# Optimization experiments

Hardware: AMD Instinct MI355X
Metric: run time of the kernel (lower is better)

The kernel has to match this reference:

```python
import jax, jax.numpy as jnp
import numpy as np

B, T, C, H = 4, 1024, 2048, 16
HD = C // H  # head_dim = 128


def setup_inputs() -> dict:
    key = jax.random.key(0)
    k1, k2, k3 = jax.random.split(key, 3)
    x = jax.random.normal(k1, (B, T, C), dtype=jnp.float32)
    # torch Linear weights are [out_features, in_features]
    w_attn = jax.random.normal(k2, (3 * C, C), dtype=jnp.float32) * 0.02
    w_proj = jax.random.normal(k3, (C, C), dtype=jnp.float32) * 0.02
    attention_mask = jnp.ones((B, T), dtype=jnp.int32)  # 1 = attend, 0 = padded
    return {"x": x, "w_attn": w_attn, "w_proj": w_proj, "attention_mask": attention_mask}


def reference(x, w_attn, w_proj, attention_mask):
    b, t, c = x.shape
    hd = c // H
    # fused QKV projection: [B,T,3C] -> [3,B,H,T,hd]
    qkv = jnp.einsum("btc,fc->btf", x, w_attn)
    qkv = qkv.reshape(b, t, 3, H, hd).transpose(2, 0, 3, 1, 4)
    q, k, v = qkv[0], qkv[1], qkv[2]
    # padding mask -> additive bias, broadcast over heads and query positions
    bias = jnp.where(attention_mask == 0, -jnp.inf, 0.0).astype(x.dtype)[:, None, None, :]
    scale = 1.0 / jnp.sqrt(jnp.asarray(hd, dtype=x.dtype))
    att = jnp.einsum("bhqd,bhkd->bhqk", q, k) * scale + bias
    att = jax.nn.softmax(att, axis=-1)  # dropout_p=0 (eval mode)
    y = jnp.einsum("bhqk,bhkd->bhqd", att, v)
    y = y.transpose(0, 2, 1, 3).reshape(b, t, c)
    return jnp.einsum("btc,oc->bto", y, w_proj)
```

## Files before the change

kernel.cpp:

```cpp
#include <hip/hip_runtime.h>
#include <hip/hip_bf16.h>

#define NB   4
#define NH   16
#define SEQ  1024
#define CH   2048
#define HDIM 128

typedef float f32x4 __attribute__((ext_vector_type(4)));
typedef short short8 __attribute__((ext_vector_type(8)));

static __device__ __forceinline__ unsigned short f2bf(float f) {
  unsigned u = __builtin_bit_cast(unsigned, f);
  u += 0x7FFFu + ((u >> 16) & 1u);
  return (unsigned short)(u >> 16);
}

#define GLOAD16(g, l)                                                        \
  __builtin_amdgcn_global_load_lds(                                          \
      (const __attribute__((address_space(1))) void*)(g),                    \
      (__attribute__((address_space(3))) void*)(l), 16, 0, 0)

__global__ __launch_bounds__(256)
void cast_bf16(const float* __restrict__ in, unsigned short* __restrict__ out, int n4) {
  int i = blockIdx.x * 256 + threadIdx.x;
  int stride = gridDim.x * 256;
  for (; i < n4; i += stride) {
    float4 v = ((const float4*)in)[i];
    ushort4 o;
    o.x = f2bf(v.x); o.y = f2bf(v.y); o.z = f2bf(v.z); o.w = f2bf(v.w);
    ((ushort4*)out)[i] = o;
  }
}

__device__ __forceinline__ void gemm_core_glds(
    const unsigned short* __restrict__ A, const unsigned short* __restrict__ B,
    int K, int m0, int n0, short* As, short* Bs, f32x4 acc[4][4]) {
  const int tid = threadIdx.x, lane = tid & 63, wid = tid >> 6;
  const int wr = wid >> 1, wc = wid & 1, lr = lane & 15, lg = lane >> 4;
  const int sr = lane >> 3;
  const int sk = (lane & 7) * 8;

  for (int k0 = 0; k0 < K; k0 += 64) {
    __syncthreads();
#pragma unroll
    for (int p = 0; p < 4; ++p) {
      int c = wid * 4 + p;
      GLOAD16(A + (size_t)(m0 + c * 8 + sr) * K + k0 + sk, As + c * 512);
      GLOAD16(B + (size_t)(n0 + c * 8 + sr) * K + k0 + sk, Bs + c * 512);
    }
    __syncthreads();
#pragma unroll
    for (int kc = 0; kc < 2; ++kc) {
      short8 af[4], bf[4];
#pragma unroll
      for (int f = 0; f < 4; ++f) {
        af[f] = *(const short8*)(As + (wr * 64 + f * 16 + lr) * 64 + kc * 32 + lg * 8);
        bf[f] = *(const short8*)(Bs + (wc * 64 + f * 16 + lr) * 64 + kc * 32 + lg * 8);
      }
#pragma unroll
      for (int fm = 0; fm < 4; ++fm)
#pragma unroll
        for (int fn = 0; fn < 4; ++fn)
          acc[fm][fn] = __builtin_amdgcn_mfma_f32_16x16x32_bf16(af[fm], bf[fn], acc[fm][fn], 0, 0, 0);
    }
  }
  __syncthreads();
}

__global__ __launch_bounds__(256)
void gemm_qkv_bf16(const unsigned short* __restrict__ xb, const unsigned short* __restrict__ wab,
                   unsigned short* __restrict__ Qb, unsigned short* __restrict__ Kb,
                   unsigned short* __restrict__ Vtb) {
  __shared__ short smem[17408];
  short* As = smem;
  short* Bs = smem + 8192;
  f32x4 acc[4][4];
#pragma unroll
  for (int i = 0; i < 4; ++i)
#pragma unroll
    for (int j = 0; j < 4; ++j) acc[i][j] = (f32x4){0.f, 0.f, 0.f, 0.f};

  const int m0 = blockIdx.y * 128, n0 = blockIdx.x * 128;
  gemm_core_glds(xb, wab, CH, m0, n0, As, Bs, acc);

  const int tid = threadIdx.x, lane = tid & 63, wid = tid >> 6;
  const int wr = wid >> 1, wc = wid & 1, lr = lane & 15, lg = lane >> 4;
  const int which = n0 >> 11;
  const int h = (n0 >> 7) & 15;
  const int bb = m0 >> 10, t0 = m0 & 1023;

  if (which < 2) {
    unsigned short* dst0 = (which == 0) ? Qb : Kb;
    const float sc = (which == 0) ? 0.08838834764831843f : 1.0f;
#pragma unroll
    for (int fm = 0; fm < 4; ++fm)
#pragma unroll
      for (int fn = 0; fn < 4; ++fn)
#pragma unroll
        for (int r = 0; r < 4; ++r)
          smem[(wr * 64 + fm * 16 + lg * 4 + r) * 136 + wc * 64 + fn * 16 + lr] =
              (short)f2bf(acc[fm][fn][r] * sc);
    __syncthreads();
    int row = tid >> 1, sg = tid & 1;
    unsigned short* dst = dst0 + (((size_t)(bb * NH + h)) * SEQ + t0 + row) * HDIM + sg * 64;
    const short* src = smem + row * 136 + sg * 64;
#pragma unroll
    for (int j = 0; j < 8; ++j)
      *(uint4*)(dst + j * 8) = *(const uint4*)(src + j * 8);
  } else {
#pragma unroll
    for (int fm = 0; fm < 4; ++fm)
#pragma unroll
      for (int fn = 0; fn < 4; ++fn)
#pragma unroll
        for (int r = 0; r < 4; ++r)
          smem[(wc * 64 + fn * 16 + lr) * 136 + wr * 64 + fm * 16 + lg * 4 + r] =
              (short)f2bf(acc[fm][fn][r]);
    __syncthreads();
    int dd = tid >> 1, sg = tid & 1;
    unsigned short* gdst = Vtb + (((size_t)(bb * NH + h)) * HDIM + dd) * SEQ + t0 + sg * 64;
    const short* src = smem + dd * 136 + sg * 64;
#pragma unroll
    for (int j = 0; j < 8; ++j)
      *(uint4*)(gdst + j * 8) = *(const uint4*)(src + j * 8);
  }
}

__global__ __launch_bounds__(256)
void gemm_proj_bf16(const unsigned short* __restrict__ Yb, const unsigned short* __restrict__ wpb,
                    float* __restrict__ out) {
  __shared__ short smem[17408];
  short* As = smem;
  short* Bs = smem + 8192;
  f32x4 acc[4][4];
#pragma unroll
  for (int i = 0; i < 4; ++i)
#pragma unroll
    for (int j = 0; j < 4; ++j) acc[i][j] = (f32x4){0.f, 0.f, 0.f, 0.f};

  const int m0 = blockIdx.y * 128, n0 = blockIdx.x * 128;
  gemm_core_glds(Yb, wpb, CH, m0, n0, As, Bs, acc);

  const int tid = threadIdx.x, lane = tid & 63, wid = tid >> 6;
  const int wr = wid >> 1, wc = wid & 1, lr = lane & 15, lg = lane >> 4;
  float* fb = (float*)smem;
  for (int p = 0; p < 2; ++p) {
    if (wr == p) {
#pragma unroll
      for (int fm = 0; fm < 4; ++fm)
#pragma unroll
        for (int fn = 0; fn < 4; ++fn)
#pragma unroll
          for (int r = 0; r < 4; ++r)
            fb[(fm * 16 + lg * 4 + r) * 132 + wc * 64 + fn * 16 + lr] = acc[fm][fn][r];
    }
    __syncthreads();
    int row = tid >> 2, seg = tid & 3;
    float* dst = out + (size_t)(m0 + p * 64 + row) * CH + n0 + seg * 32;
    const float* src = fb + row * 132 + seg * 32;
#pragma unroll
    for (int j = 0; j < 8; ++j)
      *(uint4*)(dst + j * 4) = *(const uint4*)(src + j * 4);
    __syncthreads();
  }
}

__global__ __launch_bounds__(256)
void attn_mfma(const unsigned short* __restrict__ Qb, const unsigned short* __restrict__ Kb,
               const unsigned short* __restrict__ Vtb, const int* __restrict__ mask,
               unsigned short* __restrict__ Yb) {
  __shared__ short asmem[12032];
  short* Kls = asmem;
  short* Vls = asmem + 4352;
  short* Pls = asmem + 9472;
  const int tid = threadIdx.x, lane = tid & 63, wid = tid >> 6;
  const int lr = lane & 15, lg = lane >> 4;
  const int bh = blockIdx.y, b = bh >> 4, h = bh & 15;
  const int q0 = blockIdx.x * 64 + wid * 16;

  short8 qf[4];
  const unsigned short* qptr = Qb + ((size_t)bh * SEQ + q0 + lr) * HDIM + lg * 8;
#pragma unroll
  for (int dc = 0; dc < 4; ++dc) qf[dc] = *(const short8*)(qptr + dc * 32);

  f32x4 O[8];
#pragma unroll
  for (int i = 0; i < 8; ++i) O[i] = (f32x4){0.f, 0.f, 0.f, 0.f};
  float mrow[4] = {-3.0e38f, -3.0e38f, -3.0e38f, -3.0e38f};
  float lrow[4] = {0.f, 0.f, 0.f, 0.f};

  const unsigned short* kbase = Kb + (size_t)bh * SEQ * HDIM;
  const unsigned short* vbase = Vtb + (size_t)bh * HDIM * SEQ;
  short* Pw = Pls + wid * (16 * 40);
  const int* maskrow = mask + b * SEQ;

  for (int kt = 0; kt < SEQ; kt += 32) {
    __syncthreads();
    {
      int r = tid >> 3, s = tid & 7;
      const unsigned short* g = kbase + (size_t)(kt + r) * HDIM + s * 16;
      uint4 u0 = *(const uint4*)g, u1 = *(const uint4*)(g + 8);
      *(uint4*)(Kls + r * 136 + s * 16) = u0;
      *(uint4*)(Kls + r * 136 + s * 16 + 8) = u1;
      int d = tid >> 1, s2 = tid & 1;
      const unsigned short* gv = vbase + (size_t)d * SEQ + kt + s2 * 16;
      uint4 v0 = *(const uint4*)gv, v1 = *(const uint4*)(gv + 8);
      *(uint4*)(Vls + d * 40 + s2 * 16) = v0;
      *(uint4*)(Vls + d * 40 + s2 * 16 + 8) = v1;
    }
    __syncthreads();

    f32x4 s0 = (f32x4){0.f, 0.f, 0.f, 0.f}, s1 = (f32x4){0.f, 0.f, 0.f, 0.f};
#pragma unroll
    for (int dc = 0; dc < 4; ++dc) {
      short8 k0f = *(const short8*)(Kls + lr * 136 + dc * 32 + lg * 8);
      short8 k1f = *(const short8*)(Kls + (16 + lr) * 136 + dc * 32 + lg * 8);
      s0 = __builtin_amdgcn_mfma_f32_16x16x32_bf16(qf[dc], k0f, s0, 0, 0, 0);
      s1 = __builtin_amdgcn_mfma_f32_16x16x32_bf16(qf[dc], k1f, s1, 0, 0, 0);
    }

    float b0 = maskrow[kt + lr] ? 0.f : -1.0e30f;
    float b1 = maskrow[kt + 16 + lr] ? 0.f : -1.0e30f;
    float corr[4];
#pragma unroll
    for (int r = 0; r < 4; ++r) {
      float a0 = s0[r] + b0, a1 = s1[r] + b1;
      float tm = fmaxf(a0, a1);
      tm = fmaxf(tm, __shfl_xor(tm, 1));
      tm = fmaxf(tm, __shfl_xor(tm, 2));
      tm = fmaxf(tm, __shfl_xor(tm, 4));
      tm = fmaxf(tm, __shfl_xor(tm, 8));
      float mn = fmaxf(mrow[r], tm);
      corr[r] = __expf(mrow[r] - mn);
      float p0 = __expf(a0 - mn), p1 = __expf(a1 - mn);
      mrow[r] = mn;
      float rs = p0 + p1;
      rs += __shfl_xor(rs, 1);
      rs += __shfl_xor(rs, 2);
      rs += __shfl_xor(rs, 4);
      rs += __shfl_xor(rs, 8);
      lrow[r] = lrow[r] * corr[r] + rs;
      Pw[(lg * 4 + r) * 40 + lr] = (short)f2bf(p0);
      Pw[(lg * 4 + r) * 40 + 16 + lr] = (short)f2bf(p1);
    }
#pragma unroll
    for (int db = 0; db < 8; ++db)
#pragma unroll
      for (int r = 0; r < 4; ++r) O[db][r] *= corr[r];

    short8 pa = *(const short8*)(Pw + lr * 40 + lg * 8);
#pragma unroll
    for (int db = 0; db < 8; ++db) {
      short8 vb = *(const short8*)(Vls + (db * 16 + lr) * 40 + lg * 8);
      O[db] = __builtin_amdgcn_mfma_f32_16x16x32_bf16(pa, vb, O[db], 0, 0, 0);
    }
  }

  float inv[4];
#pragma unroll
  for (int r = 0; r < 4; ++r) inv[r] = 1.0f / lrow[r];

  short* Ols = asmem;
  __syncthreads();
#pragma unroll
  for (int db = 0; db < 8; ++db)
#pragma unroll
    for (int r = 0; r < 4; ++r)
      Ols[(wid * 16 + lg * 4 + r) * 136 + db * 16 + lr] = (short)f2bf(O[db][r] * inv[r]);
  __syncthreads();
  {
    int row = tid >> 2, seg = tid & 3;
    unsigned short* dst =
        Yb + ((size_t)(b * SEQ + blockIdx.x * 64 + row)) * CH + h * HDIM + seg * 32;
    const short* src = Ols + row * 136 + seg * 32;
#pragma unroll
    for (int j = 0; j < 4; ++j)
      *(uint4*)(dst + j * 8) = *(const uint4*)(src + j * 8);
  }
}

extern "C" void kernel_launch(void* const* d_in, const int* in_sizes, int n_in,
                              void* d_out, int out_size, void* d_ws, size_t ws_size,
                              hipStream_t stream) {
  const float* x      = (const float*)d_in[0];
  const float* w_attn = (const float*)d_in[1];
  const float* w_proj = (const float*)d_in[2];
  const int*   mask   = (const int*)d_in[3];
  float* out = (float*)d_out;

  char* ws = (char*)d_ws;
  unsigned short* xb  = (unsigned short*)(ws);
  unsigned short* wab = (unsigned short*)(ws + 16777216);
  unsigned short* wpb = (unsigned short*)(ws + 41943040);
  unsigned short* Qb  = (unsigned short*)(ws + 50331648);
  unsigned short* Kb  = (unsigned short*)(ws + 67108864);
  unsigned short* Vtb = (unsigned short*)(ws + 83886080);
  unsigned short* Yb  = (unsigned short*)(ws + 100663296);

  cast_bf16<<<2048, 256, 0, stream>>>(x, xb, (NB * SEQ * CH) / 4);
  cast_bf16<<<2048, 256, 0, stream>>>(w_attn, wab, (3 * CH * CH) / 4);
  cast_bf16<<<2048, 256, 0, stream>>>(w_proj, wpb, (CH * CH) / 4);

  gemm_qkv_bf16<<<dim3(3 * CH / 128, NB * SEQ / 128), 256, 0, stream>>>(xb, wab, Qb, Kb, Vtb);
  attn_mfma<<<dim3(SEQ / 64, NB * NH), 256, 0, stream>>>(Qb, Kb, Vtb, mask, Yb);
  gemm_proj_bf16<<<dim3(CH / 128, NB * SEQ / 128), 256, 0, stream>>>(Yb, wpb, out);
}
```

Before: 470.6 us.

## Replace QKV GEMM with 256x256 double-buffered tile kernel and block swizzle

The QKV projection now uses a new kernel with 256x256 output tiles and 512 threads (8 waves, 8x4 MFMA fragments each). A/B tiles are staged with direct global-to-LDS loads into two LDS buffers, so the next K-slice is fetched while the current one is computed. A linear block-index swizzle groups neighbouring tiles for better L2 reuse. Larger tiles cut global/LDS traffic per FLOP. In exchange the kernel uses 128KB of LDS (one block per CU), launches only 384 blocks, which may leave a partial wave, and the epilogue runs in two serialized halves.

```diff
diff --git a/kernel.cpp b/kernel.cpp
--- a/kernel.cpp
+++ b/kernel.cpp
@@ -33,6 +33,119 @@
   }
 }
 
+__global__ __launch_bounds__(512, 2)
+void gemm_qkv_256(const unsigned short* __restrict__ xb, const unsigned short* __restrict__ wab,
+                  unsigned short* __restrict__ Qb, unsigned short* __restrict__ Kb,
+                  unsigned short* __restrict__ Vtb) {
+  __shared__ short smem[65536];
+  const int tid = threadIdx.x, lane = tid & 63, wid = tid >> 6;
+  const int wr = wid >> 2, wc = wid & 3, lr = lane & 15, lg = lane >> 4;
+  const int sr = lane >> 3, sk = (lane & 7) * 8;
+
+  const int lid = blockIdx.y * 24 + blockIdx.x;
+  const int swz = (lid & 7) * 48 + (lid >> 3);
+  const int bx = swz % 24, by = swz / 24;
+  const int m0 = by * 256, n0 = bx * 256;
+
+  f32x4 acc[8][4];
+#pragma unroll
+  for (int i = 0; i < 8; ++i)
+#pragma unroll
+    for (int j = 0; j < 4; ++j) acc[i][j] = (f32x4){0.f, 0.f, 0.f, 0.f};
+
+#define STAGE_TILE(b, k0)                                                      \
+  do {                                                                         \
+    short* As_ = smem + (b) * 32768;                                           \
+    short* Bs_ = As_ + 16384;                                                  \
+    _Pragma("unroll")                                                          \
+    for (int p = 0; p < 4; ++p) {                                              \
+      int c = wid * 4 + p;                                                     \
+      GLOAD16(xb + (size_t)(m0 + c * 8 + sr) * CH + (k0) + sk, As_ + c * 512); \
+      GLOAD16(wab + (size_t)(n0 + c * 8 + sr) * CH + (k0) + sk, Bs_ + c * 512);\
+    }                                                                          \
+  } while (0)
+
+  STAGE_TILE(0, 0);
+  __syncthreads();
+  int cur = 0;
+  for (int kt = 0; kt < 32; ++kt) {
+    if (kt + 1 < 32) STAGE_TILE(cur ^ 1, (kt + 1) * 64);
+    const short* As = smem + cur * 32768;
+    const short* Bs = As + 16384;
+#pragma unroll
+    for (int kc = 0; kc < 2; ++kc) {
+      short8 bfr[4];
+#pragma unroll
+      for (int fn = 0; fn < 4; ++fn)
+        bfr[fn] = *(const short8*)(Bs + (wc * 64 + fn * 16 + lr) * 64 + kc * 32 + lg * 8);
+#pragma unroll
+      for (int fm = 0; fm < 8; ++fm) {
+        short8 af = *(const short8*)(As + (wr * 128 + fm * 16 + lr) * 64 + kc * 32 + lg * 8);
+#pragma unroll
+        for (int fn = 0; fn < 4; ++fn)
+          acc[fm][fn] = __builtin_amdgcn_mfma_f32_16x16x32_bf16(af, bfr[fn], acc[fm][fn], 0, 0, 0);
+      }
+    }
+    __syncthreads();
+    cur ^= 1;
+  }
+#undef STAGE_TILE
+
+  const int which = n0 >> 11;
+  const int h0 = (n0 & 2047) >> 7;
+  const int bb = m0 >> 10, t0 = m0 & 1023;
+
+  if (which < 2) {
+    unsigned short* dst0 = (which == 0) ? Qb : Kb;
+    const float sc = (which == 0) ? 0.08838834764831843f : 1.0f;
+    for (int p = 0; p < 2; ++p) {
+      if (wr == p) {
+#pragma unroll
+        for (int fm = 0; fm < 8; ++fm)
+#pragma unroll
+          for (int fn = 0; fn < 4; ++fn)
+#pragma unroll
+            for (int r = 0; r < 4; ++r)
+              smem[(fm * 16 + lg * 4 + r) * 264 + wc * 64 + fn * 16 + lr] =
+                  (short)f2bf(acc[fm][fn][r] * sc);
+      }
+      __syncthreads();
+      int row = tid >> 2, seg = tid & 3;
+      int h = h0 + (seg >> 1), d0 = (seg & 1) * 64;
+      unsigned short* dst =
+          dst0 + (((size_t)(bb * NH + h)) * SEQ + t0 + p * 128 + row) * HDIM + d0;
+      const short* src = smem + row * 264 + seg * 64;
+#pragma unroll
+      for (int j = 0; j < 8; ++j)
+        *(uint4*)(dst + j * 8) = *(const uint4*)(src + j * 8);
+      __syncthreads();
+    }
+  } else {
+    for (int p = 0; p < 2; ++p) {
+      if (wr == p) {
+#pragma unroll
+        for (int fm = 0; fm < 8; ++fm)
+#pragma unroll
+          for (int fn = 0; fn < 4; ++fn)
+#pragma unroll
+            for (int r = 0; r < 4; ++r)
+              smem[(wc * 64 + fn * 16 + lr) * 136 + fm * 16 + lg * 4 + r] =
+                  (short)f2bf(acc[fm][fn][r]);
+      }
+      __syncthreads();
+      int d = tid >> 1, sg = tid & 1;
+      int h = h0 + (d >> 7), dl = d & 127;
+      unsigned short* dst =
+          Vtb + (((size_t)(bb * NH + h)) * HDIM + dl) * SEQ + t0 + p * 128 + sg * 64;
+      const short* src = smem + d * 136 + sg * 64;
+#pragma unroll
+      for (int j = 0; j < 8; ++j)
+        *(uint4*)(dst + j * 8) = *(const uint4*)(src + j * 8);
+      __syncthreads();
+    }
+  }
+}
+
 __device__ __forceinline__ void gemm_core_glds(
     const unsigned short* __restrict__ A, const unsigned short* __restrict__ B,
     int K, int m0, int n0, short* As, short* Bs, f32x4 acc[4][4]) {
@@ -66,65 +179,6 @@
     }
   }
   __syncthreads();
-}
-
-__global__ __launch_bounds__(256)
-void gemm_qkv_bf16(const unsigned short* __restrict__ xb, const unsigned short* __restrict__ wab,
-                   unsigned short* __restrict__ Qb, unsigned short* __restrict__ Kb,
-                   unsigned short* __restrict__ Vtb) {
-  __shared__ short smem[17408];
-  short* As = smem;
-  short* Bs = smem + 8192;
-  f32x4 acc[4][4];
-#pragma unroll
-  for (int i = 0; i < 4; ++i)
-#pragma unroll
-    for (int j = 0; j < 4; ++j) acc[i][j] = (f32x4){0.f, 0.f, 0.f, 0.f};
-
-  const int m0 = blockIdx.y * 128, n0 = blockIdx.x * 128;
-  gemm_core_glds(xb, wab, CH, m0, n0, As, Bs, acc);
-
-  const int tid = threadIdx.x, lane = tid & 63, wid = tid >> 6;
-  const int wr = wid >> 1, wc = wid & 1, lr = lane & 15, lg = lane >> 4;
-  const int which = n0 >> 11;
-  const int h = (n0 >> 7) & 15;
-  const int bb = m0 >> 10, t0 = m0 & 1023;
-
-  if (which < 2) {
-    unsigned short* dst0 = (which == 0) ? Qb : Kb;
-    const float sc = (which == 0) ? 0.08838834764831843f : 1.0f;
-#pragma unroll
-    for (int fm = 0; fm < 4; ++fm)
-#pragma unroll
-      for (int fn = 0; fn < 4; ++fn)
-#pragma unroll
-        for (int r = 0; r < 4; ++r)
-          smem[(wr * 64 + fm * 16 + lg * 4 + r) * 136 + wc * 64 + fn * 16 + lr] =
-              (short)f2bf(acc[fm][fn][r] * sc);
-    __syncthreads();
-    int row = tid >> 1, sg = tid & 1;
-    unsigned short* dst = dst0 + (((size_t)(bb * NH + h)) * SEQ + t0 + row) * HDIM + sg * 64;
-    const short* src = smem + row * 136 + sg * 64;
-#pragma unroll
-    for (int j = 0; j < 8; ++j)
-      *(uint4*)(dst + j * 8) = *(const uint4*)(src + j * 8);
-  } else {
-#pragma unroll
-    for (int fm = 0; fm < 4; ++fm)
-#pragma unroll
-      for (int fn = 0; fn < 4; ++fn)
-#pragma unroll
-        for (int r = 0; r < 4; ++r)
-          smem[(wc * 64 + fn * 16 + lr) * 136 + wr * 64 + fm * 16 + lg * 4 + r] =
-              (short)f2bf(acc[fm][fn][r]);
-    __syncthreads();
-    int dd = tid >> 1, sg = tid & 1;
-    unsigned short* gdst = Vtb + (((size_t)(bb * NH + h)) * HDIM + dd) * SEQ + t0 + sg * 64;
-    const short* src = smem + dd * 136 + sg * 64;
-#pragma unroll
-    for (int j = 0; j < 8; ++j)
-      *(uint4*)(gdst + j * 8) = *(const uint4*)(src + j * 8);
-  }
 }
 
 __global__ __launch_bounds__(256)
@@ -302,7 +356,7 @@
   cast_bf16<<<2048, 256, 0, stream>>>(w_attn, wab, (3 * CH * CH) / 4);
   cast_bf16<<<2048, 256, 0, stream>>>(w_proj, wpb, (CH * CH) / 4);
 
-  gemm_qkv_bf16<<<dim3(3 * CH / 128, NB * SEQ / 128), 256, 0, stream>>>(xb, wab, Qb, Kb, Vtb);
+  gemm_qkv_256<<<dim3(24, 16), 512, 0, stream>>>(xb, wab, Qb, Kb, Vtb);
   attn_mfma<<<dim3(SEQ / 64, NB * NH), 256, 0, stream>>>(Qb, Kb, Vtb, mask, Yb);
   gemm_proj_bf16<<<dim3(CH / 128, NB * SEQ / 128), 256, 0, stream>>>(Yb, wpb, out);
 }
```

After: 466.7 us. About the same (-0.8%).
